# Performance work log

Measured on AMD Instinct MI355X. Metric: run time of the kernel, lower is better.

The kernel has to match this reference:

```python
import jax, jax.numpy as jnp
import numpy as np

B, L, D_MODEL = 2, 2048, 1024
EXPAND, D_STATE, D_CONV = 2, 16, 4
D_INNER = EXPAND * D_MODEL          # 2048
DT_RANK = D_MODEL // 16             # 64 (mamba-ssm 'auto' rank)


def setup_inputs() -> dict:
    key = jax.random.key(0)
    ks = jax.random.split(key, 8)
    s = lambda k, shape, scale: jax.random.normal(k, shape, jnp.float32) * scale
    x = s(ks[0], (B, L, D_MODEL), 1.0)
    W_in = s(ks[1], (2 * D_INNER, D_MODEL), D_MODEL ** -0.5)
    conv_w = s(ks[2], (D_INNER, 1, D_CONV), D_CONV ** -0.5)   # depthwise kernel
    conv_b = s(ks[3], (D_INNER,), 0.02)
    W_xproj = s(ks[4], (DT_RANK + 2 * D_STATE, D_INNER), D_INNER ** -0.5)
    W_dt = s(ks[5], (D_INNER, DT_RANK), DT_RANK ** -0.5)
    # inverse-softplus of dt ~= 0.01 (mamba default dt init region)
    b_dt = jnp.log(jnp.expm1(0.01 * jnp.ones((D_INNER,), jnp.float32)))
    # S4D-real init: A = -[1..d_state] per channel
    A_log = jnp.log(jnp.broadcast_to(
        jnp.arange(1, D_STATE + 1, dtype=jnp.float32), (D_INNER, D_STATE)))
    D = jnp.ones((D_INNER,), jnp.float32)
    W_out = s(ks[6], (D_MODEL, D_INNER), D_INNER ** -0.5)
    return dict(x=x, W_in=W_in, conv_w=conv_w, conv_b=conv_b, W_xproj=W_xproj,
                W_dt=W_dt, b_dt=b_dt, A_log=A_log, D=D, W_out=W_out)


def reference(x, W_in, conv_w, conv_b, W_xproj, W_dt, b_dt, A_log, D, W_out):
    # in_proj: [B,L,d_model] -> [B,L,2*d_inner]
    xz = jnp.einsum('bld,ed->ble', x, W_in)
    xs, z = jnp.split(xz, 2, axis=-1)

    # causal depthwise conv1d over time, kernel d_conv
    xc = jnp.swapaxes(xs, 1, 2)  # [B, d_inner, L]
    xc = jax.lax.conv_general_dilated(
        xc, conv_w, window_strides=(1,), padding=[(D_CONV - 1, 0)],
        feature_group_count=D_INNER)
    xc = xc + conv_b[None, :, None]
    xs = jax.nn.silu(jnp.swapaxes(xc, 1, 2))  # [B,L,d_inner]

    # x_proj -> (dt, B, C)
    x_dbl = jnp.einsum('bld,ed->ble', xs, W_xproj)
    dt, Bm, Cm = jnp.split(x_dbl, [DT_RANK, DT_RANK + D_STATE], axis=-1)
    dt = jax.nn.softplus(jnp.einsum('blr,dr->bld', dt, W_dt) + b_dt)  # [B,L,d_inner]

    A = -jnp.exp(A_log)  # [d_inner, d_state]

    def step(h, inp):
        dt_t, B_t, C_t, x_t = inp  # [B,d], [B,n], [B,n], [B,d]
        dA = jnp.exp(dt_t[..., None] * A)                       # [B,d,n]
        h = h * dA + (dt_t * x_t)[..., None] * B_t[:, None, :]  # [B,d,n]
        y = jnp.einsum('bdn,bn->bd', h, C_t)
        return h, y

    tm = lambda a: jnp.swapaxes(a, 0, 1)  # time-major for scan
    h0 = jnp.zeros((x.shape[0], D_INNER, D_STATE), x.dtype)
    _, ys = jax.lax.scan(step, h0, (tm(dt), tm(Bm), tm(Cm), tm(xs)))

    y = tm(ys) + xs * D          # skip term D*x
    y = y * jax.nn.silu(z)       # gate
    return jnp.einsum('bld,ed->ble', y, W_out)  # out_proj -> [B,L,d_model]
```

## Files before the change

kernel.cpp:

```cpp
#include <hip/hip_runtime.h>
#include <cstdint>
#include <cstddef>

typedef __bf16 bf16_t;
typedef bf16_t bf16x4 __attribute__((ext_vector_type(4)));
typedef bf16_t bf16x8 __attribute__((ext_vector_type(8)));
typedef float f32x4 __attribute__((ext_vector_type(4)));

static __device__ __forceinline__ void glds16(const void* g, void* l) {
    __builtin_amdgcn_global_load_lds((const __attribute__((address_space(1))) void*)g,
                                     (__attribute__((address_space(3))) void*)l,
                                     16, 0, 0);
}

#define BARRIER()  asm volatile("s_barrier" ::: "memory")
#define DS_WAIT()  do { asm volatile("s_waitcnt lgkmcnt(0)" ::: "memory"); \
                        __builtin_amdgcn_sched_barrier(0); } while (0)

__global__ __launch_bounds__(256)
void cast5(const float* __restrict__ s0, bf16_t* __restrict__ d0, int n0,
           const float* __restrict__ s1, bf16_t* __restrict__ d1, int n1,
           const float* __restrict__ s2, bf16_t* __restrict__ d2, int n2,
           const float* __restrict__ s3, bf16_t* __restrict__ d3, int n3,
           const float* __restrict__ s4, bf16_t* __restrict__ d4)
{
    int bb = blockIdx.x;
    const float* s; bf16_t* d;
    if (bb < n0)              { s = s0; d = d0; }
    else if ((bb -= n0) < n1) { s = s1; d = d1; }
    else if ((bb -= n1) < n2) { s = s2; d = d2; }
    else if ((bb -= n2) < n3) { s = s3; d = d3; }
    else                      { bb -= n3; s = s4; d = d4; }
    const size_t base = (size_t)bb * 1024 + threadIdx.x * 4;
    const f32x4 v = *(const f32x4*)(s + base);
    bf16x4 o;
    o[0] = (bf16_t)v[0]; o[1] = (bf16_t)v[1]; o[2] = (bf16_t)v[2]; o[3] = (bf16_t)v[3];
    *(bf16x4*)(d + base) = o;
}

#define LOAD_A(MQ) \
    _Pragma("unroll") for (int mf = 0; mf < 4; ++mf) { \
        aF[mf][0] = *(const bf16x8*)(Ab + (aRow + (MQ)*64 + mf*16)*64 + ck0); \
        aF[mf][1] = *(const bf16x8*)(Ab + (aRow + (MQ)*64 + mf*16)*64 + ck1); }

#define LOAD_B(NQ, dst) \
    _Pragma("unroll") for (int nf = 0; nf < 2; ++nf) { \
        dst[nf][0] = *(const bf16x8*)(Bb + (bRow + (NQ)*32 + nf*16)*64 + ck0); \
        dst[nf][1] = *(const bf16x8*)(Bb + (bRow + (NQ)*32 + nf*16)*64 + ck1); }

#define MFMA16(MQ, NQ, bset) \
    __builtin_amdgcn_s_setprio(1); \
    _Pragma("unroll") for (int mf = 0; mf < 4; ++mf) \
    _Pragma("unroll") for (int nf = 0; nf < 2; ++nf) \
    _Pragma("unroll") for (int kk = 0; kk < 2; ++kk) \
        acc[(MQ)*4+mf][(NQ)*2+nf] = __builtin_amdgcn_mfma_f32_16x16x32_bf16( \
            aF[mf][kk], bset[nf][kk], acc[(MQ)*4+mf][(NQ)*2+nf], 0, 0, 0); \
    __builtin_amdgcn_s_setprio(0);

template<int EPI>
__global__ __launch_bounds__(512, 2)
void gemm256_bt(const bf16_t* __restrict__ A, const bf16_t* __restrict__ Bt,
                const int N, const int K,
                bf16_t* __restrict__ o0, bf16_t* __restrict__ o1)
{
    constexpr int TILE = 256 * 64;
    __shared__ __align__(16) bf16_t As[2 * TILE];
    __shared__ __align__(16) bf16_t Bs[2 * TILE];

    const int tid  = threadIdx.x;
    const int lane = tid & 63;
    const int w    = tid >> 6;
    const int wm   = w >> 2, wn = w & 3;
    const int l16  = lane & 15, quad = lane >> 4;
    const int e7   = l16 & 7;
    const int ck0  = (quad ^ e7) << 3;
    const int ck1  = ck0 ^ 32;
    const int lr   = lane >> 3, l8 = lane & 7;
    const int swz  = (l8 ^ lr) << 3;
    const int m0   = blockIdx.y * 256, n0 = blockIdx.x * 256;
    const int NT   = K >> 6;

    const int aRow = wm * 128 + l16;
    const int bRow = wn * 64 + l16;

    f32x4 acc[8][4] = {};
    bf16x8 aF[4][2], bLo[2][2], bHi[2][2];

    auto STAGE = [&](int unit, int kt, int d) {
        const bf16_t* g; int rg0; bf16_t* lb; int rbase;
        if (unit <= 1) { g = A;  rg0 = m0; lb = As;
                         rbase = unit * 64 + w * 8; }
        else           { g = Bt; rg0 = n0; lb = Bs;
                         rbase = ((w >> 2) << 6) + ((w & 3) << 3) + ((unit & 1) << 5); }
#pragma unroll
        for (int L = 0; L < 2; ++L) {
            const int rb = rbase + L * 128;
            glds16(g + (size_t)(rg0 + rb + lr) * K + kt * 64 + swz,
                   lb + d * TILE + rb * 64);
        }
    };

    STAGE(2, 0, 0); STAGE(0, 0, 0); STAGE(3, 0, 0); STAGE(1, 0, 0);
    if (NT > 1) { STAGE(2, 1, 1); STAGE(0, 1, 1); STAGE(3, 1, 1); }
    if (NT > 1) asm volatile("s_waitcnt vmcnt(6)" ::: "memory");
    else        asm volatile("s_waitcnt vmcnt(0)" ::: "memory");
    BARRIER();

    for (int i = 0; i < NT; ++i) {
        const int b = i & 1;
        const bf16_t* Ab = As + b * TILE;
        const bf16_t* Bb = Bs + b * TILE;

        LOAD_A(0); LOAD_B(0, bLo);
        if (i + 1 < NT) STAGE(1, i + 1, (i + 1) & 1);
        BARRIER(); DS_WAIT();
        MFMA16(0, 0, bLo);
        __builtin_amdgcn_sched_barrier(0);
        BARRIER();

        LOAD_B(1, bHi);
        if (i + 2 < NT) STAGE(2, i + 2, b);
        BARRIER(); DS_WAIT();
        MFMA16(0, 1, bHi);
        __builtin_amdgcn_sched_barrier(0);
        BARRIER();

        LOAD_A(1);
        if (i + 2 < NT) STAGE(0, i + 2, b);
        BARRIER(); DS_WAIT();
        MFMA16(1, 1, bHi);
        __builtin_amdgcn_sched_barrier(0);
        BARRIER();

        if (i + 2 < NT) STAGE(3, i + 2, b);
        BARRIER(); DS_WAIT();
        MFMA16(1, 0, bLo);
        __builtin_amdgcn_sched_barrier(0);
        if (i + 2 < NT) asm volatile("s_waitcnt vmcnt(6)" ::: "memory");
        else            asm volatile("s_waitcnt vmcnt(0)" ::: "memory");
        BARRIER();
    }

#pragma unroll
    for (int mf = 0; mf < 8; ++mf)
#pragma unroll
        for (int nf = 0; nf < 4; ++nf)
#pragma unroll
            for (int r = 0; r < 4; ++r) {
                const int gr = m0 + wm * 128 + mf * 16 + quad * 4 + r;
                const int gc = n0 + wn * 64 + nf * 16 + l16;
                const float v = acc[mf][nf][r];
                if (EPI == 1) {
                    if (gc < 2048) o0[(size_t)gr * 2048 + gc] = (bf16_t)v;
                    else           o1[(size_t)gr * 2048 + (gc - 2048)] = (bf16_t)v;
                } else {
                    ((float*)o0)[(size_t)gr * N + gc] = v;
                }
            }
}

template<int EPI, int SPLITK>
__global__ __launch_bounds__(256)
void gemm_bt(const bf16_t* __restrict__ A, const bf16_t* __restrict__ Bt,
             const int M, const int N, const int K,
             void* __restrict__ o0, void* __restrict__ o1,
             const float* __restrict__ bias,
             float* __restrict__ p0, float* __restrict__ p1,
             float* __restrict__ p2, float* __restrict__ p3)
{
    __shared__ __align__(16) bf16_t As[128 * 64];
    __shared__ __align__(16) bf16_t Bs[128 * 64];

    const int tid  = threadIdx.x;
    const int lane = tid & 63;
    const int wave = tid >> 6;
    const int wm = wave & 1, wn = wave >> 1;
    const int m0 = blockIdx.y * 128, n0 = blockIdx.x * 128;
    const int quad = lane >> 4, l16 = lane & 15;
    const int z   = (SPLITK > 1) ? blockIdx.z : 0;
    const int KC  = K / SPLITK;
    const int kb  = z * KC;

    f32x4 acc[4][4] = {};

    for (int k0 = kb; k0 < kb + KC; k0 += 64) {
        __syncthreads();
#pragma unroll
        for (int j = 0; j < 4; j++) {
            const int u  = wave * 2048 + j * 512;
            const int ue = u + lane * 8;
            const int row = ue >> 6, col = ue & 63;
            glds16(A  + (size_t)(m0 + row) * K + k0 + col, As + u);
            glds16(Bt + (size_t)(n0 + row) * K + k0 + col, Bs + u);
        }
        __syncthreads();

#pragma unroll
        for (int kk = 0; kk < 2; kk++) {
            bf16x8 afr[4], bfr[4];
#pragma unroll
            for (int mt = 0; mt < 4; mt++)
                afr[mt] = *(const bf16x8*)(As + (wm * 64 + mt * 16 + l16) * 64 + kk * 32 + quad * 8);
#pragma unroll
            for (int nt = 0; nt < 4; nt++)
                bfr[nt] = *(const bf16x8*)(Bs + (wn * 64 + nt * 16 + l16) * 64 + kk * 32 + quad * 8);
#pragma unroll
            for (int mt = 0; mt < 4; mt++)
#pragma unroll
                for (int nt = 0; nt < 4; nt++)
                    acc[mt][nt] = __builtin_amdgcn_mfma_f32_16x16x32_bf16(
                        afr[mt], bfr[nt], acc[mt][nt], 0, 0, 0);
        }
    }

    float* pz = (z == 0) ? p0 : (z == 1) ? p1 : (z == 2) ? p2 : p3;

#pragma unroll
    for (int mt = 0; mt < 4; mt++)
#pragma unroll
        for (int nt = 0; nt < 4; nt++)
#pragma unroll
            for (int r = 0; r < 4; r++) {
                const int gr = m0 + wm * 64 + mt * 16 + quad * 4 + r;
                const int gc = n0 + wn * 64 + nt * 16 + l16;
                const float v = acc[mt][nt][r];
                if (EPI == 0) {
                    ((float*)o0)[(size_t)gr * N + gc] = v;
                } else if (EPI == 1) {
                    if (gc < 2048) ((bf16_t*)o0)[(size_t)gr * 2048 + gc] = (bf16_t)v;
                    else           ((bf16_t*)o1)[(size_t)gr * 2048 + (gc - 2048)] = (bf16_t)v;
                } else if (EPI == 2) {
                    const float t  = v + bias[gc];
                    const float sp = (t > 15.f) ? t : __logf(1.f + __expf(t));
                    ((bf16_t*)o0)[(size_t)gr * 2048 + gc] = (bf16_t)sp;
                } else {
                    pz[(size_t)gr * N + gc] = v;
                }
            }
}

__global__ __launch_bounds__(256)
void reduce_k(float* __restrict__ out, const float* __restrict__ p0,
              const float* __restrict__ p1, const float* __restrict__ p2,
              const float* __restrict__ p3, const int nsplit)
{
    const size_t i = ((size_t)blockIdx.x * 256 + threadIdx.x) * 4;
    f32x4 v = *(const f32x4*)(p0 + i);
    v += *(const f32x4*)(p1 + i);
    if (nsplit == 4) {
        v += *(const f32x4*)(p2 + i);
        v += *(const f32x4*)(p3 + i);
    }
    *(f32x4*)(out + i) = v;
}

__global__ __launch_bounds__(256)
void conv_silu(const bf16_t* __restrict__ xs_pre, const float* __restrict__ cw,
               const float* __restrict__ cb, bf16_t* __restrict__ xs)
{
    const int idx = blockIdx.x * 256 + threadIdx.x;
    const int d   = idx & 2047;
    const int row = idx >> 11;
    const int l   = row & 2047;
    const float w0 = cw[d * 4 + 0], w1 = cw[d * 4 + 1];
    const float w2 = cw[d * 4 + 2], w3 = cw[d * 4 + 3];
    const bf16_t* p = xs_pre + (size_t)row * 2048 + d;
    float acc = cb[d] + w3 * (float)p[0];
    if (l >= 1) acc += w2 * (float)p[-2048];
    if (l >= 2) acc += w1 * (float)p[-4096];
    if (l >= 3) acc += w0 * (float)p[-6144];
    const float s = acc / (1.f + __expf(-acc));
    xs[idx] = (bf16_t)s;
}

__global__ __launch_bounds__(64)
void xproj_kernel(const bf16_t* __restrict__ A, const bf16_t* __restrict__ Bt,
                  bf16_t* __restrict__ dtr, float* __restrict__ Bm, float* __restrict__ Cm)
{
    const int lane = threadIdx.x;
    const int m0 = blockIdx.x * 16;
    const int l16 = lane & 15, quad = lane >> 4;
    f32x4 acc[6] = {};

    const bf16_t* ap = A + (size_t)(m0 + l16) * 2048 + quad * 8;
    for (int k0 = 0; k0 < 2048; k0 += 32) {
        const bf16x8 afr = *(const bf16x8*)(ap + k0);
#pragma unroll
        for (int t = 0; t < 6; t++) {
            const bf16x8 bfr = *(const bf16x8*)(Bt + (size_t)(t * 16 + l16) * 2048 + k0 + quad * 8);
            acc[t] = __builtin_amdgcn_mfma_f32_16x16x32_bf16(afr, bfr, acc[t], 0, 0, 0);
        }
    }
#pragma unroll
    for (int t = 0; t < 6; t++)
#pragma unroll
        for (int r = 0; r < 4; r++) {
            const int gr = m0 + quad * 4 + r;
            const int gc = t * 16 + l16;
            const float v = acc[t][r];
            if (gc < 64)      dtr[(size_t)gr * 64 + gc] = (bf16_t)v;
            else if (gc < 80) Bm[(size_t)gr * 16 + (gc - 64)] = v;
            else              Cm[(size_t)gr * 16 + (gc - 80)] = v;
        }
}

static __device__ __forceinline__ bool fast_check(const float* A_log, int d, float& a1) {
    a1 = -__expf(A_log[(size_t)d * 16]);
    bool ok = true;
#pragma unroll
    for (int n = 1; n < 16; n++) {
        const float an = -__expf(A_log[(size_t)d * 16 + n]);
        const float pn = (float)(n + 1) * a1;
        ok = ok && (fabsf(an - pn) <= 1e-3f * fabsf(pn) + 1e-6f);
    }
    return ok;
}

__global__ __launch_bounds__(256)
void scan1(const bf16_t* __restrict__ dt, const bf16_t* __restrict__ xs,
           const float* __restrict__ Bm, const float* __restrict__ A_log,
           float* __restrict__ sdt_o, bf16_t* __restrict__ Hsum)
{
    const int tid = threadIdx.x;
    const int bi  = blockIdx.x;
    const int c   = bi & 63;
    const int bb  = bi >> 6;
    const int b   = bb >> 3;
    const int d   = (bb & 7) * 256 + tid;
    float a1; const bool fast = fast_check(A_log, d, a1);

    float h[16] = {};
    float s = 0.f;
    const size_t rowbase = (size_t)b * 2048 + c * 32;

    if (fast) {
#pragma unroll 4
        for (int t = 0; t < 32; t++) {
            const size_t ro = (rowbase + t) * 2048 + d;
            const float dtv = (float)dt[ro];
            const float xv  = (float)xs[ro];
            s += dtv;
            const float r = __expf(dtv * a1);
            float rp[16]; rp[0] = r;
#pragma unroll
            for (int n = 1; n < 16; n++) rp[n] = rp[n - 1] * r;
            const float bx = dtv * xv;
            const float* bp = Bm + (rowbase + t) * 16;
#pragma unroll
            for (int n = 0; n < 16; n++) h[n] = fmaf(h[n], rp[n], bx * bp[n]);
        }
    } else {
        for (int t = 0; t < 32; t++) {
            const size_t ro = (rowbase + t) * 2048 + d;
            const float dtv = (float)dt[ro];
            const float xv  = (float)xs[ro];
            s += dtv;
            const float bx = dtv * xv;
            const float* bp = Bm + (rowbase + t) * 16;
#pragma unroll
            for (int n = 0; n < 16; n++) {
                const float an = -__expf(A_log[(size_t)d * 16 + n]);
                h[n] = fmaf(h[n], __expf(dtv * an), bx * bp[n]);
            }
        }
    }
    const size_t sb = (size_t)bi * 256 + tid;
    sdt_o[sb] = s;
    bf16x8 h0, h1;
#pragma unroll
    for (int n = 0; n < 8; n++) { h0[n] = (bf16_t)h[n]; h1[n] = (bf16_t)h[n + 8]; }
    *(bf16x8*)(Hsum + sb * 16)     = h0;
    *(bf16x8*)(Hsum + sb * 16 + 8) = h1;
}

__global__ __launch_bounds__(256)
void scan2(const float* __restrict__ sdt, bf16_t* __restrict__ Hsum,
           const float* __restrict__ A_log)
{
    const int tid = threadIdx.x;
    const int bb  = blockIdx.x;
    const int d   = (bb & 7) * 256 + tid;
    float a1; const bool fast = fast_check(A_log, d, a1);

    float h[16] = {};
    for (int c = 0; c < 64; c++) {
        const size_t sb = ((size_t)(bb * 64 + c) * 256 + tid);
        const float s = sdt[sb];
        bf16x8 hs0 = *(const bf16x8*)(Hsum + sb * 16);
        bf16x8 hs1 = *(const bf16x8*)(Hsum + sb * 16 + 8);
        bf16x8 o0, o1;
#pragma unroll
        for (int n = 0; n < 8; n++) { o0[n] = (bf16_t)h[n]; o1[n] = (bf16_t)h[n + 8]; }
        *(bf16x8*)(Hsum + sb * 16)     = o0;
        *(bf16x8*)(Hsum + sb * 16 + 8) = o1;
        if (fast) {
            const float r = __expf(s * a1);
            float rp[16]; rp[0] = r;
#pragma unroll
            for (int n = 1; n < 16; n++) rp[n] = rp[n - 1] * r;
#pragma unroll
            for (int n = 0; n < 16; n++) {
                const float hsv = (n < 8) ? (float)hs0[n] : (float)hs1[n - 8];
                h[n] = fmaf(h[n], rp[n], hsv);
            }
        } else {
#pragma unroll
            for (int n = 0; n < 16; n++) {
                const float an = -__expf(A_log[(size_t)d * 16 + n]);
                const float hsv = (n < 8) ? (float)hs0[n] : (float)hs1[n - 8];
                h[n] = fmaf(h[n], __expf(s * an), hsv);
            }
        }
    }
}

__global__ __launch_bounds__(256)
void scan3(const bf16_t* __restrict__ dt, const bf16_t* __restrict__ xs,
           bf16_t* __restrict__ zy,
           const float* __restrict__ Bm, const float* __restrict__ Cm,
           const float* __restrict__ A_log, const float* __restrict__ Dv,
           const bf16_t* __restrict__ Hseed)
{
    const int tid = threadIdx.x;
    const int bi  = blockIdx.x;
    const int c   = bi & 63;
    const int bb  = bi >> 6;
    const int b   = bb >> 3;
    const int d   = (bb & 7) * 256 + tid;
    float a1; const bool fast = fast_check(A_log, d, a1);
    const float Dd = Dv[d];

    const size_t sb = (size_t)bi * 256 + tid;
    const bf16x8 hs0 = *(const bf16x8*)(Hseed + sb * 16);
    const bf16x8 hs1 = *(const bf16x8*)(Hseed + sb * 16 + 8);
    float h[16];
#pragma unroll
    for (int n = 0; n < 8; n++) { h[n] = (float)hs0[n]; h[n + 8] = (float)hs1[n]; }

    const size_t rowbase = (size_t)b * 2048 + c * 32;

    if (fast) {
#pragma unroll 2
        for (int t = 0; t < 32; t++) {
            const size_t ro = (rowbase + t) * 2048 + d;
            const float dtv = (float)dt[ro];
            const float xv  = (float)xs[ro];
            const float zv  = (float)zy[ro];
            const float r = __expf(dtv * a1);
            float rp[16]; rp[0] = r;
#pragma unroll
            for (int n = 1; n < 16; n++) rp[n] = rp[n - 1] * r;
            const float bx = dtv * xv;
            const float* bp = Bm + (rowbase + t) * 16;
            const float* cp = Cm + (rowbase + t) * 16;
            float y0 = 0.f, y1 = 0.f;
#pragma unroll
            for (int n = 0; n < 16; n += 2) {
                h[n]     = fmaf(h[n],     rp[n],     bx * bp[n]);
                h[n + 1] = fmaf(h[n + 1], rp[n + 1], bx * bp[n + 1]);
                y0 = fmaf(h[n],     cp[n],     y0);
                y1 = fmaf(h[n + 1], cp[n + 1], y1);
            }
            const float yv = (y0 + y1) + xv * Dd;
            const float g  = zv / (1.f + __expf(-zv));
            zy[ro] = (bf16_t)(yv * g);
        }
    } else {
        for (int t = 0; t < 32; t++) {
            const size_t ro = (rowbase + t) * 2048 + d;
            const float dtv = (float)dt[ro];
            const float xv  = (float)xs[ro];
            const float zv  = (float)zy[ro];
            const float bx = dtv * xv;
            const float* bp = Bm + (rowbase + t) * 16;
            const float* cp = Cm + (rowbase + t) * 16;
            float y = 0.f;
#pragma unroll
            for (int n = 0; n < 16; n++) {
                const float an = -__expf(A_log[(size_t)d * 16 + n]);
                h[n] = fmaf(h[n], __expf(dtv * an), bx * bp[n]);
                y = fmaf(h[n], cp[n], y);
            }
            const float yv = y + xv * Dd;
            const float g  = zv / (1.f + __expf(-zv));
            zy[ro] = (bf16_t)(yv * g);
        }
    }
}

extern "C" void kernel_launch(void* const* d_in, const int* in_sizes, int n_in,
                              void* d_out, int out_size, void* d_ws, size_t ws_size,
                              hipStream_t stream)
{
    const float* x     = (const float*)d_in[0];
    const float* W_in  = (const float*)d_in[1];
    const float* convw = (const float*)d_in[2];
    const float* convb = (const float*)d_in[3];
    const float* W_xp  = (const float*)d_in[4];
    const float* W_dt  = (const float*)d_in[5];
    const float* b_dt  = (const float*)d_in[6];
    const float* A_log = (const float*)d_in[7];
    const float* Dv    = (const float*)d_in[8];
    const float* W_out = (const float*)d_in[9];

    char* ws = (char*)d_ws;
    bf16_t* bufP   = (bf16_t*)(ws + 0);
    bf16_t* bufZ   = (bf16_t*)(ws + 16777216);
    bf16_t* bufX   = (bf16_t*)(ws + 33554432);
    bf16_t* W_in_b = (bf16_t*)(ws + 33554432);
    bf16_t* dtr    = (bf16_t*)(ws + 50331648);
    float*  Bm     = (float*)(ws + 50855936);
    float*  Cm     = (float*)(ws + 51118080);
    float*  sdt    = (float*)(ws + 51380224);
    bf16_t* Hsum   = (bf16_t*)(ws + 52428800);
    bf16_t* x_b    = (bf16_t*)(ws + 52428800);
    bf16_t* W_out_b= (bf16_t*)(ws + 60817408);
    bf16_t* W_xp_b = (bf16_t*)(ws + 65011712);
    bf16_t* W_dt_b = (bf16_t*)(ws + 65404928);
    float*  P0     = (float*)(ws + 0);
    float*  P1     = (float*)(ws + 33554432);
    float*  P2     = (float*)(ws + 65667072);
    float*  P3     = (float*)(ws + 82444288);
    const bool sk4 = (ws_size >= 99221504ull);

    cast5<<<dim3(4096 + 4096 + 2048 + 192 + 128), dim3(256), 0, stream>>>(
        x, x_b, 4096, W_in, W_in_b, 4096, W_out, W_out_b, 2048,
        W_xp, W_xp_b, 192, W_dt, W_dt_b);

    gemm256_bt<1><<<dim3(16, 16), dim3(512), 0, stream>>>(
        x_b, W_in_b, 4096, 1024, bufP, bufZ);

    conv_silu<<<dim3(32768), dim3(256), 0, stream>>>(bufP, convw, convb, bufX);

    xproj_kernel<<<dim3(256), dim3(64), 0, stream>>>(bufX, W_xp_b, dtr, Bm, Cm);

    gemm_bt<2, 1><<<dim3(16, 32), dim3(256), 0, stream>>>(
        dtr, W_dt_b, 4096, 2048, 64, (void*)bufP, nullptr, b_dt,
        nullptr, nullptr, nullptr, nullptr);

    scan1<<<dim3(1024), dim3(256), 0, stream>>>(bufP, bufX, Bm, A_log, sdt, Hsum);
    scan2<<<dim3(16),   dim3(256), 0, stream>>>(sdt, Hsum, A_log);
    scan3<<<dim3(1024), dim3(256), 0, stream>>>(bufP, bufX, bufZ, Bm, Cm, A_log, Dv, Hsum);

    if (sk4) {
        gemm_bt<3, 4><<<dim3(8, 32, 4), dim3(256), 0, stream>>>(
            bufZ, W_out_b, 4096, 1024, 2048, nullptr, nullptr, nullptr,
            P0, P1, P2, P3);
        reduce_k<<<dim3(4096), dim3(256), 0, stream>>>(
            (float*)d_out, P0, P1, P2, P3, 4);
    } else {
        gemm_bt<3, 2><<<dim3(8, 32, 2), dim3(256), 0, stream>>>(
            bufZ, W_out_b, 4096, 1024, 2048, nullptr, nullptr, nullptr,
            P0, P1, nullptr, nullptr);
        reduce_k<<<dim3(4096), dim3(256), 0, stream>>>(
            (float*)d_out, P0, P1, nullptr, nullptr, 2);
    }
}
```

Measured before the change: 316.3 us.

## Use 256-tile GEMM for split-K out_proj, vectorize conv, split-K xproj, prefetch scan2

The 256x256 GEMM kernel gains a split-K path with per-split fp32 partial outputs and now handles the out_proj GEMM in place of the 128-tile kernel. Its inner loop merges the last two staging phases into one barrier region. conv_silu now has each thread process 8 channels over 8 consecutive rows with vector loads and a rolling window. xproj splits K across 4 waves and reduces through shared memory, and scan2's fast path prefetches the next chunk's inputs. Together these aim to cut launch-grid overhead, uncoalesced loads and serialized latency. They add register pressure and a possible hazard from the reduced barrier count.

```diff
diff --git a/kernel.cpp b/kernel.cpp
--- a/kernel.cpp
+++ b/kernel.cpp
@@ -57,11 +57,13 @@
             aF[mf][kk], bset[nf][kk], acc[(MQ)*4+mf][(NQ)*2+nf], 0, 0, 0); \
     __builtin_amdgcn_s_setprio(0);
 
-template<int EPI>
+template<int EPI, int SPLITK>
 __global__ __launch_bounds__(512, 2)
 void gemm256_bt(const bf16_t* __restrict__ A, const bf16_t* __restrict__ Bt,
-                const int N, const int K,
-                bf16_t* __restrict__ o0, bf16_t* __restrict__ o1)
+                const int N, const int K, const int KC,
+                bf16_t* __restrict__ o0, bf16_t* __restrict__ o1,
+                float* __restrict__ p0, float* __restrict__ p1,
+                float* __restrict__ p2, float* __restrict__ p3)
 {
     constexpr int TILE = 256 * 64;
     __shared__ __align__(16) bf16_t As[2 * TILE];
@@ -78,7 +80,10 @@
     const int lr   = lane >> 3, l8 = lane & 7;
     const int swz  = (l8 ^ lr) << 3;
     const int m0   = blockIdx.y * 256, n0 = blockIdx.x * 256;
-    const int NT   = K >> 6;
+    const int z    = (SPLITK > 1) ? blockIdx.z : 0;
+    const int NT   = KC >> 6;
+
+    if (SPLITK > 1) { A += (size_t)z * KC; Bt += (size_t)z * KC; }
 
     const int aRow = wm * 128 + l16;
     const int bRow = wn * 64 + l16;
@@ -126,14 +131,9 @@
         BARRIER();
 
         LOAD_A(1);
-        if (i + 2 < NT) STAGE(0, i + 2, b);
+        if (i + 2 < NT) { STAGE(0, i + 2, b); STAGE(3, i + 2, b); }
         BARRIER(); DS_WAIT();
         MFMA16(1, 1, bHi);
-        __builtin_amdgcn_sched_barrier(0);
-        BARRIER();
-
-        if (i + 2 < NT) STAGE(3, i + 2, b);
-        BARRIER(); DS_WAIT();
         MFMA16(1, 0, bLo);
         __builtin_amdgcn_sched_barrier(0);
         if (i + 2 < NT) asm volatile("s_waitcnt vmcnt(6)" ::: "memory");
@@ -141,6 +141,8 @@
         BARRIER();
     }
 
+    float* pz = (EPI == 3) ? ((z == 0) ? p0 : (z == 1) ? p1 : (z == 2) ? p2 : p3)
+                           : nullptr;
 #pragma unroll
     for (int mf = 0; mf < 8; ++mf)
 #pragma unroll
@@ -153,6 +155,8 @@
                 if (EPI == 1) {
                     if (gc < 2048) o0[(size_t)gr * 2048 + gc] = (bf16_t)v;
                     else           o1[(size_t)gr * 2048 + (gc - 2048)] = (bf16_t)v;
+                } else if (EPI == 3) {
+                    pz[(size_t)gr * N + gc] = v;
                 } else {
                     ((float*)o0)[(size_t)gr * N + gc] = v;
                 }
@@ -258,50 +262,93 @@
 void conv_silu(const bf16_t* __restrict__ xs_pre, const float* __restrict__ cw,
                const float* __restrict__ cb, bf16_t* __restrict__ xs)
 {
-    const int idx = blockIdx.x * 256 + threadIdx.x;
-    const int d   = idx & 2047;
-    const int row = idx >> 11;
-    const int l   = row & 2047;
-    const float w0 = cw[d * 4 + 0], w1 = cw[d * 4 + 1];
-    const float w2 = cw[d * 4 + 2], w3 = cw[d * 4 + 3];
-    const bf16_t* p = xs_pre + (size_t)row * 2048 + d;
-    float acc = cb[d] + w3 * (float)p[0];
-    if (l >= 1) acc += w2 * (float)p[-2048];
-    if (l >= 2) acc += w1 * (float)p[-4096];
-    if (l >= 3) acc += w0 * (float)p[-6144];
-    const float s = acc / (1.f + __expf(-acc));
-    xs[idx] = (bf16_t)s;
-}
-
-__global__ __launch_bounds__(64)
+    const int d0 = threadIdx.x * 8;
+    const int rg = blockIdx.x * 8;
+    float w0[8], w1[8], w2[8], w3[8], bs[8];
+#pragma unroll
+    for (int j = 0; j < 8; j++) {
+        const f32x4 wv = *(const f32x4*)(cw + (size_t)(d0 + j) * 4);
+        w0[j] = wv[0]; w1[j] = wv[1]; w2[j] = wv[2]; w3[j] = wv[3];
+        bs[j] = cb[d0 + j];
+    }
+    float p1[8], p2[8], p3[8];
+    {
+        const int r1 = (rg >= 1) ? rg - 1 : 0;
+        const int r2 = (rg >= 2) ? rg - 2 : 0;
+        const int r3 = (rg >= 3) ? rg - 3 : 0;
+        const bf16x8 v1 = *(const bf16x8*)(xs_pre + (size_t)r1 * 2048 + d0);
+        const bf16x8 v2 = *(const bf16x8*)(xs_pre + (size_t)r2 * 2048 + d0);
+        const bf16x8 v3 = *(const bf16x8*)(xs_pre + (size_t)r3 * 2048 + d0);
+#pragma unroll
+        for (int j = 0; j < 8; j++) {
+            p1[j] = (float)v1[j]; p2[j] = (float)v2[j]; p3[j] = (float)v3[j];
+        }
+    }
+#pragma unroll
+    for (int t = 0; t < 8; t++) {
+        const int r = rg + t;
+        const int l = r & 2047;
+        const float m1 = (l >= 1) ? 1.f : 0.f;
+        const float m2 = (l >= 2) ? 1.f : 0.f;
+        const float m3 = (l >= 3) ? 1.f : 0.f;
+        const bf16x8 v = *(const bf16x8*)(xs_pre + (size_t)r * 2048 + d0);
+        bf16x8 o;
+#pragma unroll
+        for (int j = 0; j < 8; j++) {
+            const float cur = (float)v[j];
+            float a = bs[j] + w3[j] * cur;
+            a += m1 * w2[j] * p1[j];
+            a += m2 * w1[j] * p2[j];
+            a += m3 * w0[j] * p3[j];
+            const float s = a / (1.f + __expf(-a));
+            o[j] = (bf16_t)s;
+            p3[j] = p2[j]; p2[j] = p1[j]; p1[j] = cur;
+        }
+        *(bf16x8*)(xs + (size_t)r * 2048 + d0) = o;
+    }
+}
+
+__global__ __launch_bounds__(256)
 void xproj_kernel(const bf16_t* __restrict__ A, const bf16_t* __restrict__ Bt,
                   bf16_t* __restrict__ dtr, float* __restrict__ Bm, float* __restrict__ Cm)
 {
-    const int lane = threadIdx.x;
+    __shared__ float red[4][64][25];
+    const int tid  = threadIdx.x;
+    const int lane = tid & 63, w = tid >> 6;
     const int m0 = blockIdx.x * 16;
     const int l16 = lane & 15, quad = lane >> 4;
     f32x4 acc[6] = {};
 
-    const bf16_t* ap = A + (size_t)(m0 + l16) * 2048 + quad * 8;
-    for (int k0 = 0; k0 < 2048; k0 += 32) {
+    const int kbase = w * 512;
+    const bf16_t* ap = A + (size_t)(m0 + l16) * 2048 + kbase + quad * 8;
+    for (int k0 = 0; k0 < 512; k0 += 32) {
         const bf16x8 afr = *(const bf16x8*)(ap + k0);
 #pragma unroll
         for (int t = 0; t < 6; t++) {
-            const bf16x8 bfr = *(const bf16x8*)(Bt + (size_t)(t * 16 + l16) * 2048 + k0 + quad * 8);
+            const bf16x8 bfr = *(const bf16x8*)(Bt + (size_t)(t * 16 + l16) * 2048 + kbase + k0 + quad * 8);
             acc[t] = __builtin_amdgcn_mfma_f32_16x16x32_bf16(afr, bfr, acc[t], 0, 0, 0);
         }
     }
 #pragma unroll
     for (int t = 0; t < 6; t++)
 #pragma unroll
-        for (int r = 0; r < 4; r++) {
-            const int gr = m0 + quad * 4 + r;
-            const int gc = t * 16 + l16;
-            const float v = acc[t][r];
-            if (gc < 64)      dtr[(size_t)gr * 64 + gc] = (bf16_t)v;
-            else if (gc < 80) Bm[(size_t)gr * 16 + (gc - 64)] = v;
-            else              Cm[(size_t)gr * 16 + (gc - 80)] = v;
-        }
+        for (int r = 0; r < 4; r++) red[w][lane][t * 4 + r] = acc[t][r];
+    __syncthreads();
+    if (w == 0) {
+#pragma unroll
+        for (int t = 0; t < 6; t++)
+#pragma unroll
+            for (int r = 0; r < 4; r++) {
+                const int j = t * 4 + r;
+                const float v = red[0][lane][j] + red[1][lane][j]
+                              + red[2][lane][j] + red[3][lane][j];
+                const int gr = m0 + quad * 4 + r;
+                const int gc = t * 16 + l16;
+                if (gc < 64)      dtr[(size_t)gr * 64 + gc] = (bf16_t)v;
+                else if (gc < 80) Bm[(size_t)gr * 16 + (gc - 64)] = v;
+                else              Cm[(size_t)gr * 16 + (gc - 80)] = v;
+            }
+    }
 }
 
 static __device__ __forceinline__ bool fast_check(const float* A_log, int d, float& a1) {
@@ -383,27 +430,46 @@
     float a1; const bool fast = fast_check(A_log, d, a1);
 
     float h[16] = {};
-    for (int c = 0; c < 64; c++) {
-        const size_t sb = ((size_t)(bb * 64 + c) * 256 + tid);
-        const float s = sdt[sb];
-        bf16x8 hs0 = *(const bf16x8*)(Hsum + sb * 16);
-        bf16x8 hs1 = *(const bf16x8*)(Hsum + sb * 16 + 8);
-        bf16x8 o0, o1;
-#pragma unroll
-        for (int n = 0; n < 8; n++) { o0[n] = (bf16_t)h[n]; o1[n] = (bf16_t)h[n + 8]; }
-        *(bf16x8*)(Hsum + sb * 16)     = o0;
-        *(bf16x8*)(Hsum + sb * 16 + 8) = o1;
-        if (fast) {
-            const float r = __expf(s * a1);
+    if (fast) {
+        size_t sb = (size_t)(bb * 64) * 256 + tid;
+        float s_cur = sdt[sb];
+        bf16x8 h0c = *(const bf16x8*)(Hsum + sb * 16);
+        bf16x8 h1c = *(const bf16x8*)(Hsum + sb * 16 + 8);
+        for (int c = 0; c < 64; c++) {
+            const size_t sbn = sb + 256;
+            float s_nxt = 0.f; bf16x8 h0n = {}, h1n = {};
+            if (c < 63) {
+                s_nxt = sdt[sbn];
+                h0n = *(const bf16x8*)(Hsum + sbn * 16);
+                h1n = *(const bf16x8*)(Hsum + sbn * 16 + 8);
+            }
+            bf16x8 o0, o1;
+#pragma unroll
+            for (int n = 0; n < 8; n++) { o0[n] = (bf16_t)h[n]; o1[n] = (bf16_t)h[n + 8]; }
+            *(bf16x8*)(Hsum + sb * 16)     = o0;
+            *(bf16x8*)(Hsum + sb * 16 + 8) = o1;
+            const float r = __expf(s_cur * a1);
             float rp[16]; rp[0] = r;
 #pragma unroll
             for (int n = 1; n < 16; n++) rp[n] = rp[n - 1] * r;
 #pragma unroll
             for (int n = 0; n < 16; n++) {
-                const float hsv = (n < 8) ? (float)hs0[n] : (float)hs1[n - 8];
+                const float hsv = (n < 8) ? (float)h0c[n] : (float)h1c[n - 8];
                 h[n] = fmaf(h[n], rp[n], hsv);
             }
-        } else {
+            sb = sbn; s_cur = s_nxt; h0c = h0n; h1c = h1n;
+        }
+    } else {
+        for (int c = 0; c < 64; c++) {
+            const size_t sb = ((size_t)(bb * 64 + c) * 256 + tid);
+            const float s = sdt[sb];
+            bf16x8 hs0 = *(const bf16x8*)(Hsum + sb * 16);
+            bf16x8 hs1 = *(const bf16x8*)(Hsum + sb * 16 + 8);
+            bf16x8 o0, o1;
+#pragma unroll
+            for (int n = 0; n < 8; n++) { o0[n] = (bf16_t)h[n]; o1[n] = (bf16_t)h[n + 8]; }
+            *(bf16x8*)(Hsum + sb * 16)     = o0;
+            *(bf16x8*)(Hsum + sb * 16 + 8) = o1;
 #pragma unroll
             for (int n = 0; n < 16; n++) {
                 const float an = -__expf(A_log[(size_t)d * 16 + n]);
@@ -527,12 +593,13 @@
         x, x_b, 4096, W_in, W_in_b, 4096, W_out, W_out_b, 2048,
         W_xp, W_xp_b, 192, W_dt, W_dt_b);
 
-    gemm256_bt<1><<<dim3(16, 16), dim3(512), 0, stream>>>(
-        x_b, W_in_b, 4096, 1024, bufP, bufZ);
-
-    conv_silu<<<dim3(32768), dim3(256), 0, stream>>>(bufP, convw, convb, bufX);
-
-    xproj_kernel<<<dim3(256), dim3(64), 0, stream>>>(bufX, W_xp_b, dtr, Bm, Cm);
+    gemm256_bt<1, 1><<<dim3(16, 16), dim3(512), 0, stream>>>(
+        x_b, W_in_b, 4096, 1024, 1024, bufP, bufZ,
+        nullptr, nullptr, nullptr, nullptr);
+
+    conv_silu<<<dim3(512), dim3(256), 0, stream>>>(bufP, convw, convb, bufX);
+
+    xproj_kernel<<<dim3(256), dim3(256), 0, stream>>>(bufX, W_xp_b, dtr, Bm, Cm);
 
     gemm_bt<2, 1><<<dim3(16, 32), dim3(256), 0, stream>>>(
         dtr, W_dt_b, 4096, 2048, 64, (void*)bufP, nullptr, b_dt,
@@ -543,8 +610,8 @@
     scan3<<<dim3(1024), dim3(256), 0, stream>>>(bufP, bufX, bufZ, Bm, Cm, A_log, Dv, Hsum);
 
     if (sk4) {
-        gemm_bt<3, 4><<<dim3(8, 32, 4), dim3(256), 0, stream>>>(
-            bufZ, W_out_b, 4096, 1024, 2048, nullptr, nullptr, nullptr,
+        gemm256_bt<3, 4><<<dim3(4, 16, 4), dim3(512), 0, stream>>>(
+            bufZ, W_out_b, 1024, 2048, 512, nullptr, nullptr,
             P0, P1, P2, P3);
         reduce_k<<<dim3(4096), dim3(256), 0, stream>>>(
             (float*)d_out, P0, P1, P2, P3, 4);
```

Measured after the change: 281.3 us. 1.12x faster.
